# Performance work log

Hardware: AMD Instinct MI355X
Metric: run time of the kernel (lower is better)

## Reference

```python
import jax, jax.numpy as jnp
import numpy as np

EMBED_DIM = 512
NUM_HEADS = 8
EPS = 1e-6


def _feature_map(x):
    # elu(x) + 1
    return jax.nn.elu(x) + 1.0


def setup_inputs() -> dict:
    key = jax.random.key(0)
    ks = jax.random.split(key, 11)
    n, s, e = 8, 8192, EMBED_DIM
    scale = 1.0 / np.sqrt(e)
    inp = {
        "query": jax.random.normal(ks[0], (n, s, e), jnp.float32),
        "key": jax.random.normal(ks[1], (n, s, e), jnp.float32),
        "value": jax.random.normal(ks[2], (n, s, e), jnp.float32),
        "Wq": jax.random.normal(ks[3], (e, e), jnp.float32) * scale,
        "bq": jnp.zeros((e,), jnp.float32),
        "Wk": jax.random.normal(ks[4], (e, e), jnp.float32) * scale,
        "bk": jnp.zeros((e,), jnp.float32),
        "Wv": jax.random.normal(ks[5], (e, e), jnp.float32) * scale,
        "bv": jnp.zeros((e,), jnp.float32),
        "Wo": jax.random.normal(ks[6], (e, e), jnp.float32) * scale,
        "bo": jnp.zeros((e,), jnp.float32),
    }
    return inp


def reference(query, key, value, Wq, bq, Wk, bk, Wv, bv, Wo, bo):
    n, s, e = query.shape
    h = NUM_HEADS
    d = e // h
    # linear projections (torch Linear: x @ W.T + b)
    q = query @ Wq.T + bq
    k = key @ Wk.T + bk
    v = value @ Wv.T + bv
    # split into heads: [n, s, h, d]
    q = q.reshape(n, s, h, d)
    k = k.reshape(n, s, h, d)
    v = v.reshape(n, s, h, d)
    Q = _feature_map(q)
    K = _feature_map(k)
    # KV: [n, h, m, d]
    KV = jnp.einsum('nshd,nshm->nhmd', K, v)
    # normalizer Z: [n, l, h]
    Z = 1.0 / (jnp.einsum('nlhd,nhd->nlh', Q, K.sum(axis=1)) + EPS)
    # output values: [n, l, h, m]
    V = jnp.einsum('nlhd,nhmd,nlh->nlhm', Q, KV, Z)
    V = V.reshape(n, s, e)
    return V @ Wo.T + bo
```

## Files before the change

### kernel.cpp

```cpp
#include <hip/hip_runtime.h>
#include <math.h>

#define EMBED 512
#define SEQ   8192
#define EPS   1e-6f

typedef __attribute__((ext_vector_type(8))) short bf16x8;
typedef __attribute__((ext_vector_type(4))) float f32x4;
typedef unsigned short ushort_t;
typedef unsigned int uint_t;

__device__ __forceinline__ ushort_t f2bf(float x) {
  uint_t b = __float_as_uint(x);
  b += 0x7fff + ((b >> 16) & 1);
  return (ushort_t)(b >> 16);
}
__device__ __forceinline__ float bf2f(ushort_t u) {
  return __uint_as_float(((uint_t)u) << 16);
}
__device__ __forceinline__ float bfhi(uint_t packed) {
  return __uint_as_float(packed & 0xffff0000u);
}
__device__ __forceinline__ float bflo(uint_t packed) {
  return __uint_as_float(packed << 16);
}

__global__ void convert_split(const float* __restrict__ x,
                              ushort_t* __restrict__ h,
                              ushort_t* __restrict__ l, int n4) {
  const int stride = gridDim.x * blockDim.x;
  for (int i = blockIdx.x * blockDim.x + threadIdx.x; i < n4; i += stride) {
    float4 v = ((const float4*)x)[i];
    ushort_t h0 = f2bf(v.x), h1 = f2bf(v.y), h2 = f2bf(v.z), h3 = f2bf(v.w);
    ushort_t l0 = f2bf(v.x - bf2f(h0)), l1 = f2bf(v.y - bf2f(h1));
    ushort_t l2 = f2bf(v.z - bf2f(h2)), l3 = f2bf(v.w - bf2f(h3));
    uint2 hv, lv;
    hv.x = (uint_t)h0 | ((uint_t)h1 << 16); hv.y = (uint_t)h2 | ((uint_t)h3 << 16);
    lv.x = (uint_t)l0 | ((uint_t)l1 << 16); lv.y = (uint_t)l2 | ((uint_t)l3 << 16);
    ((uint2*)h)[i] = hv; ((uint2*)l)[i] = lv;
  }
}

template <bool ACT, bool SPLIT_OUT>
__global__ __launch_bounds__(256) void gemm_split(
    const ushort_t* __restrict__ Ah, const ushort_t* __restrict__ Al,
    const ushort_t* __restrict__ Bh, const ushort_t* __restrict__ Bl,
    const float* __restrict__ bias,
    ushort_t* __restrict__ Ch, ushort_t* __restrict__ Cl,
    float* __restrict__ Cf, int M) {
  __shared__ __align__(16) ushort_t lAh[128 * 32];
  __shared__ __align__(16) ushort_t lAl[128 * 32];
  __shared__ __align__(16) ushort_t lBh[128 * 32];
  __shared__ __align__(16) ushort_t lBl[128 * 32];

  const int t = threadIdx.x;
  const int m0 = blockIdx.x * 128;
  const int n0 = blockIdx.y * 128;
  const int w = t >> 6, lane = t & 63;
  const int wr = w >> 1, wc = w & 1;
  const int fl = lane & 15, kb = lane >> 4;

  f32x4 acc[4][4];
#pragma unroll
  for (int mi = 0; mi < 4; ++mi)
#pragma unroll
    for (int ni = 0; ni < 4; ++ni) acc[mi][ni] = (f32x4){0.f, 0.f, 0.f, 0.f};

  for (int kt = 0; kt < EMBED / 32; ++kt) {
#pragma unroll
    for (int j = 0; j < 2; ++j) {
      const int i = t + j * 256;
      const int r = i >> 2, p = i & 3;
      const int c = p ^ ((r >> 1) & 3);
      const size_t ga = (size_t)(m0 + r) * EMBED + kt * 32 + c * 8;
      const size_t gb = (size_t)(n0 + r) * EMBED + kt * 32 + c * 8;
      __builtin_amdgcn_global_load_lds(
          (const __attribute__((address_space(1))) void*)(const void*)&Ah[ga],
          (__attribute__((address_space(3))) void*)(void*)&lAh[(size_t)i * 8], 16, 0, 0);
      __builtin_amdgcn_global_load_lds(
          (const __attribute__((address_space(1))) void*)(const void*)&Al[ga],
          (__attribute__((address_space(3))) void*)(void*)&lAl[(size_t)i * 8], 16, 0, 0);
      __builtin_amdgcn_global_load_lds(
          (const __attribute__((address_space(1))) void*)(const void*)&Bh[gb],
          (__attribute__((address_space(3))) void*)(void*)&lBh[(size_t)i * 8], 16, 0, 0);
      __builtin_amdgcn_global_load_lds(
          (const __attribute__((address_space(1))) void*)(const void*)&Bl[gb],
          (__attribute__((address_space(3))) void*)(void*)&lBl[(size_t)i * 8], 16, 0, 0);
    }
    __syncthreads();

    bf16x8 fah[4], fal[4], fbh[4], fbl[4];
#pragma unroll
    for (int mi = 0; mi < 4; ++mi) {
      const int r = wr * 64 + mi * 16 + fl;
      const int p = kb ^ ((r >> 1) & 3);
      const int off = r * 32 + p * 8;
      fah[mi] = *(const bf16x8*)&lAh[off];
      fal[mi] = *(const bf16x8*)&lAl[off];
    }
#pragma unroll
    for (int ni = 0; ni < 4; ++ni) {
      const int r = wc * 64 + ni * 16 + fl;
      const int p = kb ^ ((r >> 1) & 3);
      const int off = r * 32 + p * 8;
      fbh[ni] = *(const bf16x8*)&lBh[off];
      fbl[ni] = *(const bf16x8*)&lBl[off];
    }
#pragma unroll
    for (int mi = 0; mi < 4; ++mi)
#pragma unroll
      for (int ni = 0; ni < 4; ++ni) {
        acc[mi][ni] = __builtin_amdgcn_mfma_f32_16x16x32_bf16(fah[mi], fbh[ni], acc[mi][ni], 0, 0, 0);
        acc[mi][ni] = __builtin_amdgcn_mfma_f32_16x16x32_bf16(fah[mi], fbl[ni], acc[mi][ni], 0, 0, 0);
        acc[mi][ni] = __builtin_amdgcn_mfma_f32_16x16x32_bf16(fal[mi], fbh[ni], acc[mi][ni], 0, 0, 0);
      }
    __syncthreads();
  }

  const int rq = lane >> 4;
#pragma unroll
  for (int mi = 0; mi < 4; ++mi)
#pragma unroll
    for (int ni = 0; ni < 4; ++ni) {
      const int col = n0 + wc * 64 + ni * 16 + fl;
      const float bv = bias[col];
#pragma unroll
      for (int q = 0; q < 4; ++q) {
        const int row = m0 + wr * 64 + mi * 16 + rq * 4 + q;
        float v = acc[mi][ni][q] + bv;
        if (ACT) v = (v > 0.f) ? (v + 1.f) : __expf(v);
        const size_t g = (size_t)row * EMBED + col;
        if (SPLIT_OUT) {
          const ushort_t hh = f2bf(v);
          Ch[g] = hh;
          Cl[g] = f2bf(v - bf2f(hh));
        } else {
          Cf[g] = v;
        }
      }
    }
}

__global__ __launch_bounds__(256) void kv_kernel(
    const ushort_t* __restrict__ Kh, const ushort_t* __restrict__ Kl,
    const ushort_t* __restrict__ Vh, const ushort_t* __restrict__ Vl,
    float* __restrict__ KV, float* __restrict__ Ksum) {
  const int nh = blockIdx.x;
  const int n = nh >> 3, h = nh & 7;
  const int sbeg = blockIdx.y * 256;
  __shared__ float Ks[32][64];
  __shared__ float Vs[32][64];
  const int t = threadIdx.x;
  const int ty = t >> 4, tx = t & 15;
  float acc[4][4] = {};
  float ks[4] = {};

  for (int s0 = 0; s0 < 256; s0 += 32) {
#pragma unroll
    for (int i = 0; i < 2; ++i) {
      const int f = t + i * 256;
      const int r = f >> 4, cg = (f & 15) * 4;
      const size_t g = ((size_t)(n * SEQ + sbeg + s0 + r)) * EMBED + h * 64 + cg;
      uint2 kh = *(const uint2*)&Kh[g], kl = *(const uint2*)&Kl[g];
      uint2 vh = *(const uint2*)&Vh[g], vl = *(const uint2*)&Vl[g];
      Ks[r][cg + 0] = bflo(kh.x) + bflo(kl.x);
      Ks[r][cg + 1] = bfhi(kh.x) + bfhi(kl.x);
      Ks[r][cg + 2] = bflo(kh.y) + bflo(kl.y);
      Ks[r][cg + 3] = bfhi(kh.y) + bfhi(kl.y);
      Vs[r][cg + 0] = bflo(vh.x) + bflo(vl.x);
      Vs[r][cg + 1] = bfhi(vh.x) + bfhi(vl.x);
      Vs[r][cg + 2] = bflo(vh.y) + bflo(vl.y);
      Vs[r][cg + 3] = bfhi(vh.y) + bfhi(vl.y);
    }
    __syncthreads();
#pragma unroll 8
    for (int s = 0; s < 32; ++s) {
      float4 vv = *(float4*)&Vs[s][ty * 4];
      float4 kk = *(float4*)&Ks[s][tx * 4];
      float v4[4] = {vv.x, vv.y, vv.z, vv.w};
      float k4[4] = {kk.x, kk.y, kk.z, kk.w};
#pragma unroll
      for (int i = 0; i < 4; ++i)
#pragma unroll
        for (int j = 0; j < 4; ++j) acc[i][j] = fmaf(v4[i], k4[j], acc[i][j]);
      if (ty == 0) {
#pragma unroll
        for (int j = 0; j < 4; ++j) ks[j] += k4[j];
      }
    }
    __syncthreads();
  }
  float* kvb = &KV[(size_t)nh * 4096];
#pragma unroll
  for (int i = 0; i < 4; ++i)
#pragma unroll
    for (int j = 0; j < 4; ++j)
      atomicAdd(&kvb[(ty * 4 + i) * 64 + tx * 4 + j], acc[i][j]);
  if (ty == 0) {
#pragma unroll
    for (int j = 0; j < 4; ++j) atomicAdd(&Ksum[nh * 64 + tx * 4 + j], ks[j]);
  }
}

__global__ __launch_bounds__(256) void stage3_kernel(
    const ushort_t* __restrict__ Qh, const ushort_t* __restrict__ Ql,
    const float* __restrict__ KV, const float* __restrict__ Ksum,
    ushort_t* __restrict__ VoH, ushort_t* __restrict__ VoL) {
  const int nh = blockIdx.x;
  const int n = nh >> 3, h = nh & 7;
  __shared__ float KVs[64][65];
  __shared__ float Qs[64][65];
  __shared__ float Ksums[64];
  __shared__ float zs[64];
  const int t = threadIdx.x;

#pragma unroll
  for (int i = 0; i < 16; ++i) {
    const int idx = t + i * 256;
    KVs[idx >> 6][idx & 63] = KV[(size_t)nh * 4096 + idx];
  }
  if (t < 64) Ksums[t] = Ksum[nh * 64 + t];
  __syncthreads();

  const int w = t >> 6, lane = t & 63;
  for (int c = 0; c < 4; ++c) {
    const int l0 = blockIdx.y * 256 + c * 64;
#pragma unroll
    for (int i = 0; i < 16; ++i) {
      const int idx = t + i * 256;
      const int r = idx >> 6, d = idx & 63;
      const size_t g = (size_t)(n * SEQ + l0 + r) * EMBED + h * 64 + d;
      Qs[r][d] = bf2f(Qh[g]) + bf2f(Ql[g]);
    }
    __syncthreads();
    if (t < 64) {
      float sum = 0.f;
#pragma unroll
      for (int d = 0; d < 64; ++d) sum = fmaf(Qs[t][d], Ksums[d], sum);
      zs[t] = 1.f / (sum + EPS);
    }
    __syncthreads();
#pragma unroll 1
    for (int rr = 0; rr < 16; ++rr) {
      const int l = w * 16 + rr;
      const float z = zs[l];
      float sum = 0.f;
#pragma unroll
      for (int d = 0; d < 64; ++d) sum = fmaf(Qs[l][d], KVs[lane][d], sum);
      const float v = z * sum;
      const size_t g = (size_t)(n * SEQ + l0 + l) * EMBED + h * 64 + lane;
      const ushort_t hh = f2bf(v);
      VoH[g] = hh;
      VoL[g] = f2bf(v - bf2f(hh));
    }
    __syncthreads();
  }
}

extern "C" void kernel_launch(void* const* d_in, const int* in_sizes, int n_in,
                              void* d_out, int out_size, void* d_ws,
                              size_t ws_size, hipStream_t stream) {
  const float* query = (const float*)d_in[0];
  const float* key   = (const float*)d_in[1];
  const float* value = (const float*)d_in[2];
  const float* Wq = (const float*)d_in[3];
  const float* bq = (const float*)d_in[4];
  const float* Wk = (const float*)d_in[5];
  const float* bk = (const float*)d_in[6];
  const float* Wv = (const float*)d_in[7];
  const float* bv = (const float*)d_in[8];
  const float* Wo = (const float*)d_in[9];
  const float* bo = (const float*)d_in[10];

  const int M = in_sizes[0] / EMBED;
  const size_t ME = (size_t)M * EMBED;

  ushort_t* S1h = (ushort_t*)d_ws;  ushort_t* S1l = S1h + ME;
  ushort_t* S2h = S1h + 2 * ME;     ushort_t* S2l = S1h + 3 * ME;
  ushort_t* S3h = S1h + 4 * ME;     ushort_t* S3l = S1h + 5 * ME;
  float* KV   = (float*)(S1h + 6 * ME);
  float* Ksum = KV + 64 * 64 * 64;
  ushort_t* Wh = (ushort_t*)(Ksum + 64 * 64);
  ushort_t* Wl = Wh + (size_t)EMBED * EMBED;

  hipMemsetAsync(KV, 0, (64 * 64 * 64 + 64 * 64) * sizeof(float), stream);

  const int n4big = (int)(ME / 4);
  const int n4w = EMBED * EMBED / 4;
  dim3 gg(M / 128, EMBED / 128);

  convert_split<<<2048, 256, 0, stream>>>(key, S1h, S1l, n4big);
  convert_split<<<256, 256, 0, stream>>>(Wk, Wh, Wl, n4w);
  gemm_split<true, true><<<gg, 256, 0, stream>>>(S1h, S1l, Wh, Wl, bk, S2h, S2l, nullptr, M);

  convert_split<<<2048, 256, 0, stream>>>(value, S1h, S1l, n4big);
  convert_split<<<256, 256, 0, stream>>>(Wv, Wh, Wl, n4w);
  gemm_split<false, true><<<gg, 256, 0, stream>>>(S1h, S1l, Wh, Wl, bv, S3h, S3l, nullptr, M);

  kv_kernel<<<dim3(64, 32), 256, 0, stream>>>(S2h, S2l, S3h, S3l, KV, Ksum);

  convert_split<<<2048, 256, 0, stream>>>(query, S1h, S1l, n4big);
  convert_split<<<256, 256, 0, stream>>>(Wq, Wh, Wl, n4w);
  gemm_split<true, true><<<gg, 256, 0, stream>>>(S1h, S1l, Wh, Wl, bq, S2h, S2l, nullptr, M);

  stage3_kernel<<<dim3(64, 32), 256, 0, stream>>>(S2h, S2l, KV, Ksum, S3h, S3l);

  convert_split<<<256, 256, 0, stream>>>(Wo, Wh, Wl, n4w);
  gemm_split<false, false><<<gg, 256, 0, stream>>>(S3h, S3l, Wh, Wl, bo, nullptr, nullptr, (float*)d_out, M);
}
```

Measured before the change: 1.315 ms.

## Rewrite stage3 as split-bf16 MFMA GEMM with fused Ksum normalizer column

Replaces the scalar FP32 LDS-based stage3 kernel with an MFMA GEMM that multiplies Q tiles by a per-head B matrix. A new prep kernel builds that matrix from KV and Ksum, converting it to hi/lo bf16 and padding it to 80 columns. Ksum sits in the extra column, so the normalizer denominator falls out of the same MFMAs and is broadcast with a shuffle. This removes the slow per-lane FP32 dot products and the serial Z computation, at the cost of one extra small launch and the approximation error of the 3-term split-bf16 product.

```diff
diff --git a/kernel.cpp b/kernel.cpp
--- a/kernel.cpp
+++ b/kernel.cpp
@@ -24,6 +24,11 @@
 __device__ __forceinline__ float bflo(uint_t packed) {
   return __uint_as_float(packed << 16);
 }
+
+#define GLL(srcp, dstp)                                                       \
+  __builtin_amdgcn_global_load_lds(                                           \
+      (const __attribute__((address_space(1))) void*)(const void*)(srcp),     \
+      (__attribute__((address_space(3))) void*)(void*)(dstp), 16, 0, 0)
 
 __global__ void convert_split(const float* __restrict__ x,
                               ushort_t* __restrict__ h,
@@ -74,18 +79,10 @@
       const int c = p ^ ((r >> 1) & 3);
       const size_t ga = (size_t)(m0 + r) * EMBED + kt * 32 + c * 8;
       const size_t gb = (size_t)(n0 + r) * EMBED + kt * 32 + c * 8;
-      __builtin_amdgcn_global_load_lds(
-          (const __attribute__((address_space(1))) void*)(const void*)&Ah[ga],
-          (__attribute__((address_space(3))) void*)(void*)&lAh[(size_t)i * 8], 16, 0, 0);
-      __builtin_amdgcn_global_load_lds(
-          (const __attribute__((address_space(1))) void*)(const void*)&Al[ga],
-          (__attribute__((address_space(3))) void*)(void*)&lAl[(size_t)i * 8], 16, 0, 0);
-      __builtin_amdgcn_global_load_lds(
-          (const __attribute__((address_space(1))) void*)(const void*)&Bh[gb],
-          (__attribute__((address_space(3))) void*)(void*)&lBh[(size_t)i * 8], 16, 0, 0);
-      __builtin_amdgcn_global_load_lds(
-          (const __attribute__((address_space(1))) void*)(const void*)&Bl[gb],
-          (__attribute__((address_space(3))) void*)(void*)&lBl[(size_t)i * 8], 16, 0, 0);
+      GLL(&Ah[ga], &lAh[(size_t)i * 8]);
+      GLL(&Al[ga], &lAl[(size_t)i * 8]);
+      GLL(&Bh[gb], &lBh[(size_t)i * 8]);
+      GLL(&Bl[gb], &lBl[(size_t)i * 8]);
     }
     __syncthreads();
 
@@ -202,58 +199,105 @@
   }
 }
 
-__global__ __launch_bounds__(256) void stage3_kernel(
+__global__ __launch_bounds__(256) void prep_b2(
+    const float* __restrict__ KV, const float* __restrict__ Ksum,
+    ushort_t* __restrict__ B2h, ushort_t* __restrict__ B2l) {
+  const int nh = blockIdx.x;
+  for (int idx = threadIdx.x; idx < 80 * 64; idx += 256) {
+    const int r = idx >> 6, d = idx & 63;
+    float val = 0.f;
+    if (r < 64) val = KV[(size_t)nh * 4096 + r * 64 + d];
+    else if (r == 64) val = Ksum[nh * 64 + d];
+    const ushort_t hh = f2bf(val);
+    B2h[(size_t)nh * 5120 + idx] = hh;
+    B2l[(size_t)nh * 5120 + idx] = f2bf(val - bf2f(hh));
+  }
+}
+
+__global__ __launch_bounds__(256) void stage3_gemm(
     const ushort_t* __restrict__ Qh, const ushort_t* __restrict__ Ql,
-    const float* __restrict__ KV, const float* __restrict__ Ksum,
+    const ushort_t* __restrict__ B2h, const ushort_t* __restrict__ B2l,
     ushort_t* __restrict__ VoH, ushort_t* __restrict__ VoL) {
-  const int nh = blockIdx.x;
+  __shared__ __align__(16) ushort_t lAh[128 * 64];
+  __shared__ __align__(16) ushort_t lAl[128 * 64];
+  const int t = threadIdx.x;
+  const int nh = blockIdx.y;
   const int n = nh >> 3, h = nh & 7;
-  __shared__ float KVs[64][65];
-  __shared__ float Qs[64][65];
-  __shared__ float Ksums[64];
-  __shared__ float zs[64];
-  const int t = threadIdx.x;
-
-#pragma unroll
-  for (int i = 0; i < 16; ++i) {
-    const int idx = t + i * 256;
-    KVs[idx >> 6][idx & 63] = KV[(size_t)nh * 4096 + idx];
-  }
-  if (t < 64) Ksums[t] = Ksum[nh * 64 + t];
+  const int l0 = blockIdx.x * 128;
+  const int w = t >> 6, lane = t & 63;
+  const int fl = lane & 15, kb = lane >> 4;
+
+#pragma unroll
+  for (int j = 0; j < 4; ++j) {
+    const int i = t + j * 256;
+    const int r = i >> 3, p = i & 7;
+    const int c = p ^ (r & 7);
+    const size_t g = (size_t)(n * SEQ + l0 + r) * EMBED + h * 64 + c * 8;
+    GLL(&Qh[g], &lAh[(size_t)i * 8]);
+    GLL(&Ql[g], &lAl[(size_t)i * 8]);
+  }
+
+  bf16x8 fbh[2][5], fbl[2][5];
+#pragma unroll
+  for (int ks = 0; ks < 2; ++ks)
+#pragma unroll
+    for (int ni = 0; ni < 5; ++ni) {
+      const size_t g = (size_t)nh * 5120 + (ni * 16 + fl) * 64 + ks * 32 + kb * 8;
+      fbh[ks][ni] = *(const bf16x8*)&B2h[g];
+      fbl[ks][ni] = *(const bf16x8*)&B2l[g];
+    }
+
+  f32x4 acc[2][5];
+#pragma unroll
+  for (int mi = 0; mi < 2; ++mi)
+#pragma unroll
+    for (int ni = 0; ni < 5; ++ni) acc[mi][ni] = (f32x4){0.f, 0.f, 0.f, 0.f};
+
   __syncthreads();
 
-  const int w = t >> 6, lane = t & 63;
-  for (int c = 0; c < 4; ++c) {
-    const int l0 = blockIdx.y * 256 + c * 64;
-#pragma unroll
-    for (int i = 0; i < 16; ++i) {
-      const int idx = t + i * 256;
-      const int r = idx >> 6, d = idx & 63;
-      const size_t g = (size_t)(n * SEQ + l0 + r) * EMBED + h * 64 + d;
-      Qs[r][d] = bf2f(Qh[g]) + bf2f(Ql[g]);
-    }
-    __syncthreads();
-    if (t < 64) {
-      float sum = 0.f;
-#pragma unroll
-      for (int d = 0; d < 64; ++d) sum = fmaf(Qs[t][d], Ksums[d], sum);
-      zs[t] = 1.f / (sum + EPS);
-    }
-    __syncthreads();
-#pragma unroll 1
-    for (int rr = 0; rr < 16; ++rr) {
-      const int l = w * 16 + rr;
-      const float z = zs[l];
-      float sum = 0.f;
-#pragma unroll
-      for (int d = 0; d < 64; ++d) sum = fmaf(Qs[l][d], KVs[lane][d], sum);
-      const float v = z * sum;
-      const size_t g = (size_t)(n * SEQ + l0 + l) * EMBED + h * 64 + lane;
-      const ushort_t hh = f2bf(v);
-      VoH[g] = hh;
-      VoL[g] = f2bf(v - bf2f(hh));
-    }
-    __syncthreads();
+#pragma unroll
+  for (int ks = 0; ks < 2; ++ks) {
+    bf16x8 fah[2], fal[2];
+#pragma unroll
+    for (int mi = 0; mi < 2; ++mi) {
+      const int r = w * 32 + mi * 16 + fl;
+      const int c = ks * 4 + kb;
+      const int p = c ^ (r & 7);
+      const int off = r * 64 + p * 8;
+      fah[mi] = *(const bf16x8*)&lAh[off];
+      fal[mi] = *(const bf16x8*)&lAl[off];
+    }
+#pragma unroll
+    for (int mi = 0; mi < 2; ++mi)
+#pragma unroll
+      for (int ni = 0; ni < 5; ++ni) {
+        acc[mi][ni] = __builtin_amdgcn_mfma_f32_16x16x32_bf16(fah[mi], fbh[ks][ni], acc[mi][ni], 0, 0, 0);
+        acc[mi][ni] = __builtin_amdgcn_mfma_f32_16x16x32_bf16(fah[mi], fbl[ks][ni], acc[mi][ni], 0, 0, 0);
+        acc[mi][ni] = __builtin_amdgcn_mfma_f32_16x16x32_bf16(fal[mi], fbh[ks][ni], acc[mi][ni], 0, 0, 0);
+      }
+  }
+
+  const int rq = lane >> 4;
+#pragma unroll
+  for (int mi = 0; mi < 2; ++mi) {
+    float zin[4];
+#pragma unroll
+    for (int q = 0; q < 4; ++q) {
+      const float den = __shfl(acc[mi][4][q], lane & 48);
+      zin[q] = 1.f / (den + EPS);
+    }
+#pragma unroll
+    for (int ni = 0; ni < 4; ++ni)
+#pragma unroll
+      for (int q = 0; q < 4; ++q) {
+        const int row = l0 + w * 32 + mi * 16 + rq * 4 + q;
+        const int col = h * 64 + ni * 16 + fl;
+        const float v = acc[mi][ni][q] * zin[q];
+        const size_t g = (size_t)(n * SEQ + row) * EMBED + col;
+        const ushort_t hh = f2bf(v);
+        VoH[g] = hh;
+        VoL[g] = f2bf(v - bf2f(hh));
+      }
   }
 }
 
@@ -282,6 +326,8 @@
   float* Ksum = KV + 64 * 64 * 64;
   ushort_t* Wh = (ushort_t*)(Ksum + 64 * 64);
   ushort_t* Wl = Wh + (size_t)EMBED * EMBED;
+  ushort_t* B2h = S1h;
+  ushort_t* B2l = S1h + (size_t)64 * 5120;
 
   hipMemsetAsync(KV, 0, (64 * 64 * 64 + 64 * 64) * sizeof(float), stream);
 
@@ -303,7 +349,8 @@
   convert_split<<<256, 256, 0, stream>>>(Wq, Wh, Wl, n4w);
   gemm_split<true, true><<<gg, 256, 0, stream>>>(S1h, S1l, Wh, Wl, bq, S2h, S2l, nullptr, M);
 
-  stage3_kernel<<<dim3(64, 32), 256, 0, stream>>>(S2h, S2l, KV, Ksum, S3h, S3l);
+  prep_b2<<<64, 256, 0, stream>>>(KV, Ksum, B2h, B2l);
+  stage3_gemm<<<dim3(SEQ / 128, 64), 256, 0, stream>>>(S2h, S2l, B2h, B2l, S3h, S3l);
 
   convert_split<<<256, 256, 0, stream>>>(Wo, Wh, Wl, n4w);
   gemm_split<false, false><<<gg, 256, 0, stream>>>(S3h, S3l, Wh, Wl, bo, nullptr, nullptr, (float*)d_out, M);
```

Result: faster. 1.220 ms (-7.2%).
